# Kernel optimization log

Measured on AMD Instinct MI355X. Metric: run time of the kernel, lower is better.

## Reference

```python
import jax, jax.numpy as jnp
import numpy as np

B, T, V, D = 64, 2048, 32000, 256  # batch, seq_len, vocab, emb_dim == hidden_size
H = D
NUM_CLASSES = 27
N_NODES = 128


def setup_inputs() -> dict:
    key = jax.random.key(0)
    ks = jax.random.split(key, 8)
    s = 1.0 / np.sqrt(D)
    return {
        "tokens": jax.random.randint(ks[0], (B, T), 0, V),
        "node_token_span_starts": jax.random.randint(ks[1], (B, N_NODES), 0, T),
        "node_token_span_ends": jax.random.randint(ks[2], (B, N_NODES), 0, T),
        "embed": jax.random.normal(ks[3], (V, D), dtype=jnp.float32),
        "Wi": jax.random.normal(ks[4], (D, 4 * H), dtype=jnp.float32) * s,
        "Wh": jax.random.normal(ks[5], (H, 4 * H), dtype=jnp.float32) * s,
        "bh": jnp.zeros((4 * H,), dtype=jnp.float32),
        "Wo": jax.random.normal(ks[6], (H, NUM_CLASSES), dtype=jnp.float32) * s,
        "bo": jnp.zeros((NUM_CLASSES,), dtype=jnp.float32),
    }


def reference(tokens, node_token_span_starts, node_token_span_ends,
              embed, Wi, Wh, bh, Wo, bo):
    # node_token_span_* are unused by the original forward (dead code).
    x = embed[tokens.astype(jnp.int32)]            # [B, T, D]
    # Precompute input projections for all timesteps in one big GEMM.
    zx = jnp.einsum('btd,df->btf', x, Wi) + bh     # [B, T, 4H]
    batch = tokens.shape[0]
    c0 = jnp.zeros((batch, H), dtype=x.dtype)
    h0 = jnp.zeros((batch, H), dtype=x.dtype)

    def step(carry, zxt):
        c, h = carry
        z = zxt + h @ Wh                           # [B, 4H]
        i, f, g, o = jnp.split(z, 4, axis=-1)
        c = jax.nn.sigmoid(f) * c + jax.nn.sigmoid(i) * jnp.tanh(g)
        h = jax.nn.sigmoid(o) * jnp.tanh(c)
        return (c, h), h

    (c, h), _ = jax.lax.scan(step, (c0, h0), jnp.swapaxes(zx, 0, 1))
    # forward_outputs[:, -1, :] == final hidden state h
    return h @ Wo + bo                             # [B, NUM_CLASSES]
```

## Files before the change

### kernel.cpp

```cpp
#include <hip/hip_runtime.h>
#include <hip/hip_bf16.h>
#include <stdint.h>

typedef __hip_bfloat16 bf16;
typedef __attribute__((ext_vector_type(8))) short short8;
typedef __attribute__((ext_vector_type(4))) float f32x4;
typedef __attribute__((ext_vector_type(4))) int i32x4;
typedef __attribute__((ext_vector_type(2))) int i32x2;
typedef __attribute__((ext_vector_type(4))) unsigned int u32x4;

#define NB   64
#define NT   2048
#define NV   32000
#define ND   256
#define NH4  1024
#define NCLS 27


__global__ __launch_bounds__(256) void k_cvt_embed(const float* __restrict__ e,
                                                   bf16* __restrict__ o) {
  int i = blockIdx.x * blockDim.x + threadIdx.x;
  float4 v = reinterpret_cast<const float4*>(e)[i];
  union { bf16 h[4]; uint2 u; } pk;
  pk.h[0] = __float2bfloat16(v.x);
  pk.h[1] = __float2bfloat16(v.y);
  pk.h[2] = __float2bfloat16(v.z);
  pk.h[3] = __float2bfloat16(v.w);
  reinterpret_cast<uint2*>(o)[i] = pk.u;
}

__global__ __launch_bounds__(256) void k_cvt_wi(const float* __restrict__ wi,
                                                bf16* __restrict__ wit) {
  int i = blockIdx.x * blockDim.x + threadIdx.x;
  int col = i >> 8;
  int k   = i & 255;
  wit[i] = __float2bfloat16(wi[k * NH4 + col]);
}

__global__ __launch_bounds__(256) void k_scale(const float* __restrict__ wh,
                                               float* __restrict__ dq,
                                               float* __restrict__ rdq,
                                               float* __restrict__ rw) {
  int col = blockIdx.x * 256 + threadIdx.x;
  float m = 0.f;
  for (int k = 0; k < ND; ++k) m = fmaxf(m, fabsf(wh[k * NH4 + col]));
  dq[col]  = m * (1.f / 16129.f);
  rdq[col] = 16129.f / m;
  rw[col]  = 127.f / m;
}

__global__ __launch_bounds__(256) void k_cvt_whq(const float* __restrict__ wh,
                                                 const float* __restrict__ rw,
                                                 signed char* __restrict__ whq) {
  int idx  = blockIdx.x * 256 + threadIdx.x;
  int ii   = idx & 15;
  int lane = (idx >> 4) & 63;
  int kq   = (idx >> 10) & 3;
  int nt   = idx >> 12;
  int k   = kq * 64 + (lane >> 4) * 16 + ii;
  int col = nt * 16 + (lane & 15);
  whq[idx] = (signed char)(int)rintf(wh[k * NH4 + col] * rw[col]);
}

__global__ __launch_bounds__(256) void k_gemm_zx(const int*  __restrict__ tokens,
                                                 const bf16* __restrict__ eb,
                                                 const bf16* __restrict__ wit,
                                                 const float* __restrict__ rdq,
                                                 int* __restrict__ zxq,
                                                 int t0, int lgch) {
  __shared__ bf16 As[4 * 64 * 8];
  __shared__ bf16 Bs[4 * 64 * 8];
  int bid  = blockIdx.x;
  int nb   = bid & 15;
  int mb   = bid >> 4;
  int n0   = nb * 64;
  int tid  = threadIdx.x, lane = tid & 63, wave = tid >> 6;
  int wm   = wave >> 1, wn = wave & 1;
  int srow = tid >> 2;
  int skg  = tid & 3;

  long trow = (long)tokens[srow * NT + t0 + mb] * ND;
  const bf16* ap = eb  + trow + skg * 8;
  const bf16* bp = wit + (long)(n0 + srow) * ND + skg * 8;
  bf16* as_dst = &As[(skg * 64 + srow) * 8];
  bf16* bs_dst = &Bs[(skg * 64 + srow) * 8];

  f32x4 acc[2][2] = {};
  for (int k0 = 0; k0 < ND; k0 += 32) {
    __syncthreads();
    *(u32x4*)as_dst = *(const u32x4*)(ap + k0);
    *(u32x4*)bs_dst = *(const u32x4*)(bp + k0);
    __syncthreads();
    short8 a0 = *(const short8*)&As[((lane >> 4) * 64 + wm * 32 +  0 + (lane & 15)) * 8];
    short8 a1 = *(const short8*)&As[((lane >> 4) * 64 + wm * 32 + 16 + (lane & 15)) * 8];
    short8 b0 = *(const short8*)&Bs[((lane >> 4) * 64 + wn * 32 +  0 + (lane & 15)) * 8];
    short8 b1 = *(const short8*)&Bs[((lane >> 4) * 64 + wn * 32 + 16 + (lane & 15)) * 8];
    acc[0][0] = __builtin_amdgcn_mfma_f32_16x16x32_bf16(a0, b0, acc[0][0], 0, 0, 0);
    acc[0][1] = __builtin_amdgcn_mfma_f32_16x16x32_bf16(a0, b1, acc[0][1], 0, 0, 0);
    acc[1][0] = __builtin_amdgcn_mfma_f32_16x16x32_bf16(a1, b0, acc[1][0], 0, 0, 0);
    acc[1][1] = __builtin_amdgcn_mfma_f32_16x16x32_bf16(a1, b1, acc[1][1], 0, 0, 0);
  }

  int cb  = n0 + wn * 32 + (lane & 15);
  float rq0 = rdq[cb], rq1 = rdq[cb + 16];
  int bb = wm * 32 + (lane >> 4) * 4;
#pragma unroll
  for (int fm = 0; fm < 2; ++fm) {
    int b0r = bb + fm * 16;
    int p0  = b0r >> 1;
#pragma unroll
    for (int fn = 0; fn < 2; ++fn) {
      int col = cb + fn * 16;
      int nt  = col >> 4;
      float rq = fn ? rq1 : rq0;
      int v0 = (int)rintf(acc[fm][fn][0] * rq);
      int v1 = (int)rintf(acc[fm][fn][1] * rq);
      int v2 = (int)rintf(acc[fm][fn][2] * rq);
      int v3 = (int)rintf(acc[fm][fn][3] * rq);
      size_t base = ((size_t)(p0 << lgch) + mb) * 2048 + nt * 32 + (col & 15) * 2;
      i32x2 w01; w01[0] = v0; w01[1] = v1;
      i32x2 w23; w23[0] = v2; w23[1] = v3;
      *(i32x2*)(zxq + base) = w01;
      *(i32x2*)(zxq + base + ((size_t)1 << lgch) * 2048) = w23;
    }
  }
}

__device__ __forceinline__ float sigf(float x) {
  return __builtin_amdgcn_rcpf(1.f + __expf(-x));
}
__device__ __forceinline__ float tanh_fast(float x) {
  return 1.f - 2.f * __builtin_amdgcn_rcpf(1.f + __expf(2.f * x));
}

__global__ __launch_bounds__(512, 1) void k_lstm(const int* __restrict__ zxq,
                                                 const signed char* __restrict__ whq,
                                                 const float* __restrict__ dq,
                                                 const float* __restrict__ bh,
                                                 float* __restrict__ cst,
                                                 float* __restrict__ hst,
                                                 int t0, int tn, int lgch) {
  __shared__ int  zl[2 * 1024];
  __shared__ signed char aF[4 * 64 * 16];

  int p   = blockIdx.x;
  int tid = threadIdx.x;
  int l   = tid & 63;
  int wv  = tid >> 6;
  int l15 = l & 15, l4 = l >> 4;
  int u   = tid & 255;
  int b   = tid >> 8;

  i32x4 w[8][4];
#pragma unroll
  for (int j = 0; j < 8; ++j) {
    int nt = wv * 8 + j;
#pragma unroll
    for (int kq = 0; kq < 4; ++kq)
      w[j][kq] = *(const i32x4*)&whq[((nt * 4 + kq) * 64 + l) * 16];
  }
#pragma unroll
  for (int j = 0; j < 8; ++j)
#pragma unroll
    for (int kq = 0; kq < 4; ++kq)
      asm volatile("" : "+v"(w[j][kq]));

  float dqv[4], bhv[4];
#pragma unroll
  for (int q = 0; q < 4; ++q) { dqv[q] = dq[q * 256 + u]; bhv[q] = bh[q * 256 + u]; }
  float c = (t0 == 0) ? 0.f : cst[(p * 2 + b) * 256 + u];

  int kqu = u >> 6, lgu = (u >> 4) & 3, iiu = u & 15;

  if (tid < 256) ((i32x4*)aF)[tid] = (i32x4)0;
  __syncthreads();
  if (t0 != 0) {
    int hq = (int)rintf(hst[(p * 2 + b) * 256 + u] * 127.f);
    aF[kqu * 1024 + (b | (lgu << 4)) * 16 + iiu] = (signed char)hq;
  }
  __syncthreads();

  const int* zb = zxq + ((size_t)(p << lgch)) * 2048 + l15 * 2;
  i32x2 z0[8];
#pragma unroll
  for (int j = 0; j < 8; ++j)
    z0[j] = *(const i32x2*)(zb + (wv * 8 + j) * 32);

  for (int lt = 0; lt < tn; ++lt) {
    i32x4 a0 = *(const i32x4*)&aF[0 * 1024 + l * 16];
    i32x4 a1 = *(const i32x4*)&aF[1 * 1024 + l * 16];
    i32x4 a2 = *(const i32x4*)&aF[2 * 1024 + l * 16];
    i32x4 a3 = *(const i32x4*)&aF[3 * 1024 + l * 16];

    i32x4 acc[8];
#pragma unroll
    for (int j = 0; j < 8; ++j) {
      i32x4 zc; zc[0] = z0[j][0]; zc[1] = z0[j][1]; zc[2] = 0; zc[3] = 0;
      i32x4 t;
      t = __builtin_amdgcn_mfma_i32_16x16x64_i8(a0, w[j][0], zc, 0, 0, 0);
      t = __builtin_amdgcn_mfma_i32_16x16x64_i8(a1, w[j][1], t, 0, 0, 0);
      t = __builtin_amdgcn_mfma_i32_16x16x64_i8(a2, w[j][2], t, 0, 0, 0);
      acc[j] = __builtin_amdgcn_mfma_i32_16x16x64_i8(a3, w[j][3], t, 0, 0, 0);
    }

    if (lt + 1 < tn) {
      const int* zn = zb + (size_t)(lt + 1) * 2048;
#pragma unroll
      for (int j = 0; j < 8; ++j)
        z0[j] = *(const i32x2*)(zn + (wv * 8 + j) * 32);
    }

    if (l4 == 0) {
#pragma unroll
      for (int j = 0; j < 8; ++j) {
        int col = (wv * 8 + j) * 16 + l15;
        zl[col]        = acc[j][0];
        zl[1024 + col] = acc[j][1];
      }
    }
    __syncthreads();

    {
      float zi = (float)zl[b * 1024 +       u] * dqv[0] + bhv[0];
      float zf = (float)zl[b * 1024 + 256 + u] * dqv[1] + bhv[1];
      float zg = (float)zl[b * 1024 + 512 + u] * dqv[2] + bhv[2];
      float zo = (float)zl[b * 1024 + 768 + u] * dqv[3] + bhv[3];
      c = sigf(zf) * c + sigf(zi) * tanh_fast(zg);
      float h = sigf(zo) * tanh_fast(c);
      aF[kqu * 1024 + (b | (lgu << 4)) * 16 + iiu] =
          (signed char)(int)rintf(h * 127.f);
      if (lt == tn - 1) hst[(p * 2 + b) * 256 + u] = h;
    }
    __syncthreads();
  }

  cst[(p * 2 + b) * 256 + u] = c;
}

__global__ __launch_bounds__(64) void k_out(const float* __restrict__ hfin,
                                            const float* __restrict__ wo,
                                            const float* __restrict__ bo,
                                            float* __restrict__ y) {
  __shared__ float hsm[256];
  int b = blockIdx.x, tid = threadIdx.x;
  for (int i = tid; i < 256; i += 64) hsm[i] = hfin[b * 256 + i];
  __syncthreads();
  if (tid < NCLS) {
    float s = bo[tid];
    for (int k = 0; k < 256; ++k) s += hsm[k] * wo[k * NCLS + tid];
    y[b * NCLS + tid] = s;
  }
}

extern "C" void kernel_launch(void* const* d_in, const int* in_sizes, int n_in,
                              void* d_out, int out_size, void* d_ws, size_t ws_size,
                              hipStream_t stream) {
  const int*   tokens = (const int*)d_in[0];
  const float* embed  = (const float*)d_in[3];
  const float* wi     = (const float*)d_in[4];
  const float* wh     = (const float*)d_in[5];
  const float* bh     = (const float*)d_in[6];
  const float* wo     = (const float*)d_in[7];
  const float* bo     = (const float*)d_in[8];
  float* y = (float*)d_out;

  char* ws = (char*)d_ws;
  bf16* eb        = (bf16*)ws;        ws += (size_t)NV * ND * 2;
  bf16* wit       = (bf16*)ws;        ws += (size_t)NH4 * ND * 2;
  signed char* whq = (signed char*)ws; ws += (size_t)ND * NH4;
  float* dqv      = (float*)ws;       ws += (size_t)NH4 * 4;
  float* rdq      = (float*)ws;       ws += (size_t)NH4 * 4;
  float* rw       = (float*)ws;       ws += (size_t)NH4 * 4;
  float* cst      = (float*)ws;       ws += (size_t)NB * ND * 4;
  float* hst      = (float*)ws;       ws += (size_t)NB * ND * 4;
  size_t fixed = (size_t)(ws - (char*)d_ws);

  int CHUNK = 32, lgch = 5;
  static const int cand[]  = {512, 256, 128, 64, 32};
  static const int candl[] = {9, 8, 7, 6, 5};
  for (int ci = 0; ci < 5; ++ci) {
    size_t need = fixed + (size_t)cand[ci] * 262144;
    if (need <= ws_size) { CHUNK = cand[ci]; lgch = candl[ci]; break; }
  }
  int* zxq = (int*)ws;

  hipLaunchKernelGGL(k_cvt_embed, dim3(NV * ND / 4 / 256), dim3(256), 0, stream, embed, eb);
  hipLaunchKernelGGL(k_cvt_wi,    dim3(NH4 * ND / 256), dim3(256), 0, stream, wi, wit);
  hipLaunchKernelGGL(k_scale,     dim3(4), dim3(256), 0, stream, wh, dqv, rdq, rw);
  hipLaunchKernelGGL(k_cvt_whq,   dim3(1024), dim3(256), 0, stream, wh, rw, whq);

  for (int t0 = 0; t0 < NT; t0 += CHUNK) {
    hipLaunchKernelGGL(k_gemm_zx, dim3(CHUNK * 16), dim3(256), 0, stream,
                       tokens, eb, wit, rdq, zxq, t0, lgch);
    hipLaunchKernelGGL(k_lstm, dim3(32), dim3(512), 0, stream,
                       zxq, whq, dqv, bh, cst, hst, t0, CHUNK, lgch);
  }
  hipLaunchKernelGGL(k_out, dim3(NB), dim3(64), 0, stream, hst, wo, bo, y);
}
```

Baseline: 2.319 ms.

## Prefetch input projections two steps ahead and interleave gate LDS layout

Unrolls the recurrent loop by two with double-buffered register sets so the precomputed input projections are fetched two timesteps ahead, giving global loads more time to land before use. It also stores the four gate pre-activations for a hidden unit contiguously in shared memory so each thread reads them with a single 16-byte load instead of four scalar loads. Costs more registers, and the two-step unroll assumes an even chunk length and that reading one step beyond the chunk at the start is valid.

```diff
diff --git a/kernel.cpp b/kernel.cpp
--- a/kernel.cpp
+++ b/kernel.cpp
@@ -133,6 +133,53 @@
   return 1.f - 2.f * __builtin_amdgcn_rcpf(1.f + __expf(2.f * x));
 }
 
+#define LSTM_STEP(Z, ST)                                                        \
+  {                                                                             \
+    i32x4 a0 = *(const i32x4*)&aF[0 * 1024 + l * 16];                           \
+    i32x4 a1 = *(const i32x4*)&aF[1 * 1024 + l * 16];                           \
+    i32x4 a2 = *(const i32x4*)&aF[2 * 1024 + l * 16];                           \
+    i32x4 a3 = *(const i32x4*)&aF[3 * 1024 + l * 16];                           \
+    i32x4 acc[8];                                                               \
+    _Pragma("unroll")                                                           \
+    for (int j = 0; j < 8; ++j) {                                               \
+      i32x4 zc; zc[0] = Z[j][0]; zc[1] = Z[j][1]; zc[2] = 0; zc[3] = 0;         \
+      i32x4 t;                                                                  \
+      t = __builtin_amdgcn_mfma_i32_16x16x64_i8(a0, w[j][0], zc, 0, 0, 0);      \
+      t = __builtin_amdgcn_mfma_i32_16x16x64_i8(a1, w[j][1], t, 0, 0, 0);       \
+      t = __builtin_amdgcn_mfma_i32_16x16x64_i8(a2, w[j][2], t, 0, 0, 0);       \
+      acc[j] = __builtin_amdgcn_mfma_i32_16x16x64_i8(a3, w[j][3], t, 0, 0, 0);  \
+    }                                                                           \
+    if ((ST) + 2 < tn) {                                                        \
+      const int* zn = zb + (size_t)((ST) + 2) * 2048;                           \
+      _Pragma("unroll")                                                         \
+      for (int j = 0; j < 8; ++j)                                               \
+        Z[j] = *(const i32x2*)(zn + (wv * 8 + j) * 32);                         \
+    }                                                                           \
+    if (l4 == 0) {                                                              \
+      _Pragma("unroll")                                                         \
+      for (int j = 0; j < 8; ++j) {                                             \
+        int col = (wv * 8 + j) * 16 + l15;                                      \
+        int tt  = ((col & 255) << 2) | (col >> 8);                              \
+        zl[tt]        = acc[j][0];                                              \
+        zl[1024 + tt] = acc[j][1];                                              \
+      }                                                                         \
+    }                                                                           \
+    __syncthreads();                                                            \
+    {                                                                           \
+      i32x4 zr = *(const i32x4*)&zl[b * 1024 + u * 4];                          \
+      float zi = (float)zr[0] * dqv[0] + bhv[0];                                \
+      float zf = (float)zr[1] * dqv[1] + bhv[1];                                \
+      float zg = (float)zr[2] * dqv[2] + bhv[2];                                \
+      float zo = (float)zr[3] * dqv[3] + bhv[3];                                \
+      c = sigf(zf) * c + sigf(zi) * tanh_fast(zg);                              \
+      float h = sigf(zo) * tanh_fast(c);                                        \
+      aF[kqu * 1024 + (b | (lgu << 4)) * 16 + iiu] =                            \
+          (signed char)(int)rintf(h * 127.f);                                   \
+      if ((ST) == tn - 1) hst[(p * 2 + b) * 256 + u] = h;                       \
+    }                                                                           \
+    __syncthreads();                                                            \
+  }
+
 __global__ __launch_bounds__(512, 1) void k_lstm(const int* __restrict__ zxq,
                                                  const signed char* __restrict__ whq,
                                                  const float* __restrict__ dq,
@@ -181,57 +228,16 @@
   __syncthreads();
 
   const int* zb = zxq + ((size_t)(p << lgch)) * 2048 + l15 * 2;
-  i32x2 z0[8];
-#pragma unroll
-  for (int j = 0; j < 8; ++j)
-    z0[j] = *(const i32x2*)(zb + (wv * 8 + j) * 32);
-
-  for (int lt = 0; lt < tn; ++lt) {
-    i32x4 a0 = *(const i32x4*)&aF[0 * 1024 + l * 16];
-    i32x4 a1 = *(const i32x4*)&aF[1 * 1024 + l * 16];
-    i32x4 a2 = *(const i32x4*)&aF[2 * 1024 + l * 16];
-    i32x4 a3 = *(const i32x4*)&aF[3 * 1024 + l * 16];
-
-    i32x4 acc[8];
-#pragma unroll
-    for (int j = 0; j < 8; ++j) {
-      i32x4 zc; zc[0] = z0[j][0]; zc[1] = z0[j][1]; zc[2] = 0; zc[3] = 0;
-      i32x4 t;
-      t = __builtin_amdgcn_mfma_i32_16x16x64_i8(a0, w[j][0], zc, 0, 0, 0);
-      t = __builtin_amdgcn_mfma_i32_16x16x64_i8(a1, w[j][1], t, 0, 0, 0);
-      t = __builtin_amdgcn_mfma_i32_16x16x64_i8(a2, w[j][2], t, 0, 0, 0);
-      acc[j] = __builtin_amdgcn_mfma_i32_16x16x64_i8(a3, w[j][3], t, 0, 0, 0);
-    }
-
-    if (lt + 1 < tn) {
-      const int* zn = zb + (size_t)(lt + 1) * 2048;
-#pragma unroll
-      for (int j = 0; j < 8; ++j)
-        z0[j] = *(const i32x2*)(zn + (wv * 8 + j) * 32);
-    }
-
-    if (l4 == 0) {
-#pragma unroll
-      for (int j = 0; j < 8; ++j) {
-        int col = (wv * 8 + j) * 16 + l15;
-        zl[col]        = acc[j][0];
-        zl[1024 + col] = acc[j][1];
-      }
-    }
-    __syncthreads();
-
-    {
-      float zi = (float)zl[b * 1024 +       u] * dqv[0] + bhv[0];
-      float zf = (float)zl[b * 1024 + 256 + u] * dqv[1] + bhv[1];
-      float zg = (float)zl[b * 1024 + 512 + u] * dqv[2] + bhv[2];
-      float zo = (float)zl[b * 1024 + 768 + u] * dqv[3] + bhv[3];
-      c = sigf(zf) * c + sigf(zi) * tanh_fast(zg);
-      float h = sigf(zo) * tanh_fast(c);
-      aF[kqu * 1024 + (b | (lgu << 4)) * 16 + iiu] =
-          (signed char)(int)rintf(h * 127.f);
-      if (lt == tn - 1) hst[(p * 2 + b) * 256 + u] = h;
-    }
-    __syncthreads();
+  i32x2 zA[8], zB[8];
+#pragma unroll
+  for (int j = 0; j < 8; ++j) {
+    zA[j] = *(const i32x2*)(zb + (wv * 8 + j) * 32);
+    zB[j] = *(const i32x2*)(zb + 2048 + (wv * 8 + j) * 32);
+  }
+
+  for (int lt = 0; lt < tn; lt += 2) {
+    LSTM_STEP(zA, lt)
+    LSTM_STEP(zB, lt + 1)
   }
 
   cst[(p * 2 + b) * 256 + u] = c;
```

Result: no change. 2.281 ms (-1.6%).
